# Optimization experiments

Measured on AMD Instinct MI355X. Metric: run time of the kernel, lower is better.

Reference implementation:

```python
import jax, jax.numpy as jnp
import numpy as np

B, T, DIM, H, DH = 4, 2048, 1024, 16, 64
NEG = -1.0e9


def setup_inputs() -> dict:
    key = jax.random.key(0)
    ks = jax.random.split(key, 12)
    inner = H * DH
    s_in = 1.0 / np.sqrt(DIM)
    s_out = 1.0 / np.sqrt(inner)
    q = jax.random.normal(ks[0], (B, T, DIM), jnp.float32)
    k = jax.random.normal(ks[1], (B, T, DIM), jnp.float32)
    v = jax.random.normal(ks[2], (B, T, DIM), jnp.float32)
    # nn.Linear weights stored as [out, in]; we keep [in, out] for x @ W
    W_q = jax.random.uniform(ks[3], (DIM, inner), jnp.float32, -s_in, s_in)
    b_q = jax.random.uniform(ks[4], (inner,), jnp.float32, -s_in, s_in)
    W_k = jax.random.uniform(ks[5], (DIM, inner), jnp.float32, -s_in, s_in)
    b_k = jax.random.uniform(ks[6], (inner,), jnp.float32, -s_in, s_in)
    W_v = jax.random.uniform(ks[7], (DIM, inner), jnp.float32, -s_in, s_in)
    b_v = jax.random.uniform(ks[8], (inner,), jnp.float32, -s_in, s_in)
    W_o = jax.random.uniform(ks[9], (inner, DIM), jnp.float32, -s_out, s_out)
    b_o = jax.random.uniform(ks[10], (DIM,), jnp.float32, -s_out, s_out)
    # causal mask: True = masked (strict upper triangle), broadcastable [1,1,T,T]
    causal_mask = jnp.triu(jnp.ones((T, T), bool), k=1)[None, None]
    # context mask: True = keep; random padding pattern with col 0 always valid
    context_mask = jax.random.bernoulli(ks[11], 0.9, (B, T)).at[:, 0].set(True)
    return {"q": q, "k": k, "v": v,
            "W_q": W_q, "b_q": b_q, "W_k": W_k, "b_k": b_k,
            "W_v": W_v, "b_v": b_v, "W_o": W_o, "b_o": b_o,
            "causal_mask": causal_mask, "context_mask": context_mask}


def reference(q, k, v, W_q, b_q, W_k, b_k, W_v, b_v, W_o, b_o,
              causal_mask, context_mask):
    scale = DH ** -0.5
    split = lambda x: x.reshape(x.shape[0], x.shape[1], H, DH).transpose(0, 2, 1, 3)
    qh = split(q @ W_q + b_q)  # [b,h,t,d]
    kh = split(k @ W_k + b_k)
    vh = split(v @ W_v + b_v)
    scores = jnp.einsum('bhid,bhjd->bhij', qh * scale, kh)
    scores = jnp.where(context_mask[:, None, None, :], scores, NEG)
    scores = jnp.where(causal_mask, NEG, scores)
    probs = jax.nn.softmax(scores, axis=-1)
    out = jnp.einsum('bhij,bhjd->bhid', probs, vh)
    out = out.transpose(0, 2, 1, 3).reshape(B, T, H * DH)
    return out @ W_o + b_o
```

## Files before the change

kernel.cpp:

```cpp
#include <hip/hip_runtime.h>
#include <hip/hip_bf16.h>
#include <cstdint>
#include <cstddef>

#define DEV static __device__ __forceinline__

typedef __attribute__((ext_vector_type(8))) short short8;
typedef __attribute__((ext_vector_type(4))) short short4v;
typedef __attribute__((ext_vector_type(4))) float floatx4;

#define BB 4
#define TT 2048
#define DIMM 1024
#define HH 16
#define DHH 64
#define MM (BB*TT)
#define QBLK 128
#define NQT (TT/QBLK)
#define M0F 12.0f

DEV unsigned short f2bu(float f) {
    unsigned int u = __float_as_uint(f);
    unsigned int r = (u + 0x7fffu + ((u >> 16) & 1u)) >> 16;
    return (unsigned short)r;
}

DEV unsigned long long pack4(float a, float b, float c, float d) {
    return (unsigned long long)f2bu(a) | ((unsigned long long)f2bu(b) << 16) |
           ((unsigned long long)f2bu(c) << 32) | ((unsigned long long)f2bu(d) << 48);
}

DEV unsigned int pk2(float lo, float hi) {
    __hip_bfloat162 h = __float22bfloat162_rn(make_float2(lo, hi));
    unsigned int r;
    __builtin_memcpy(&r, &h, 4);
    return r;
}

DEV unsigned long long pk4(float a, float b, float c, float d) {
    return (unsigned long long)pk2(a, b) | ((unsigned long long)pk2(c, d) << 32);
}

DEV void gload16(const void* g, void* l) {
    __builtin_amdgcn_global_load_lds(
        (const __attribute__((address_space(1))) unsigned int*)g,
        (__attribute__((address_space(3))) unsigned int*)l, 16, 0, 0);
}

#define MFMA16(a, b, c) __builtin_amdgcn_mfma_f32_16x16x32_bf16((a), (b), (c), 0, 0, 0)

#if defined(__has_builtin)
#if __has_builtin(__builtin_amdgcn_mfma_f32_16x16x16bf16_1k)
#define HAVE_MFMA_K16 1
#endif
#endif

DEV floatx4 mfma_k16(short4v a, short4v b, floatx4 c) {
#ifdef HAVE_MFMA_K16
    return __builtin_amdgcn_mfma_f32_16x16x16bf16_1k(a, b, c, 0, 0, 0);
#else
    asm volatile("v_mfma_f32_16x16x16_bf16 %0, %1, %2, %0" : "+v"(c) : "v"(a), "v"(b));
    return c;
#endif
}

__global__ __launch_bounds__(256) void ctx_bias(const unsigned char* __restrict__ raw,
                                                float* __restrict__ out) {
    __shared__ int nz1, nz23;
    if (threadIdx.x == 0) { nz1 = 0; nz23 = 0; }
    __syncthreads();
    int a1 = 0, a23 = 0;
    for (int i = threadIdx.x; i < BB * TT; i += 256) {
        unsigned char vb = raw[i];
        int m = i & 3;
        if (vb) { if (m == 1) a1 = 1; else if (m >= 2) a23 = 1; }
    }
    if (a1) atomicOr(&nz1, 1);
    if (a23) atomicOr(&nz23, 1);
    __syncthreads();
    const int mode = nz1 ? 2 : (nz23 ? 1 : 0);
    for (int i = threadIdx.x; i < BB * TT; i += 256) {
        bool keep;
        if (mode == 2)      keep = raw[i] != 0;
        else if (mode == 0) keep = raw[(size_t)4 * i] != 0;
        else                keep = (raw[(size_t)4 * i + 2] | raw[(size_t)4 * i + 3]) != 0;
        out[i] = keep ? -M0F : -3.0e38f;
    }
}

__global__ __launch_bounds__(256) void wtrans(const float* __restrict__ W0, const float* __restrict__ W1,
                                              const float* __restrict__ W2, const float* __restrict__ W3,
                                              unsigned short* __restrict__ out) {
    const float* W = blockIdx.y == 0 ? W0 : blockIdx.y == 1 ? W1 : blockIdx.y == 2 ? W2 : W3;
    unsigned short* O = out + (size_t)blockIdx.y * DIMM * DIMM;
    const int tx = blockIdx.x & 15, ty = blockIdx.x >> 4;
    __shared__ float s[64][65];
    const int tid = threadIdx.x;
#pragma unroll
    for (int j = 0; j < 4; ++j) {
        int c = tid + 256 * j;
        int r = c >> 4, c4 = c & 15;
        float4 vv = *reinterpret_cast<const float4*>(&W[(size_t)(ty * 64 + r) * DIMM + tx * 64 + c4 * 4]);
        s[r][c4 * 4 + 0] = vv.x; s[r][c4 * 4 + 1] = vv.y;
        s[r][c4 * 4 + 2] = vv.z; s[r][c4 * 4 + 3] = vv.w;
    }
    __syncthreads();
#pragma unroll
    for (int j = 0; j < 4; ++j) {
        int c = tid + 256 * j;
        int n = c >> 4, k4 = c & 15;
        unsigned long long pk = pack4(s[k4 * 4 + 0][n], s[k4 * 4 + 1][n], s[k4 * 4 + 2][n], s[k4 * 4 + 3][n]);
        *reinterpret_cast<unsigned long long*>(&O[(size_t)(tx * 64 + n) * DIMM + ty * 64 + k4 * 4]) = pk;
    }
}

__global__ __launch_bounds__(256) void cvt_bf16(const float* __restrict__ in,
                                                unsigned short* __restrict__ out) {
    const size_t i = ((size_t)blockIdx.x * 256 + threadIdx.x) * 8;
    float4 a = *reinterpret_cast<const float4*>(&in[i]);
    float4 b = *reinterpret_cast<const float4*>(&in[i + 4]);
    unsigned long long lo = pk4(a.x, a.y, a.z, a.w);
    unsigned long long hi = pk4(b.x, b.y, b.z, b.w);
    ulonglong2 v; v.x = lo; v.y = hi;
    *reinterpret_cast<ulonglong2*>(&out[i]) = v;
}

template <int OMODE>
__global__ __launch_bounds__(256) void gemm_bf16(const unsigned short* __restrict__ Ab,
                                                 const unsigned short* __restrict__ Bt,
                                                 const float* __restrict__ bias,
                                                 void* __restrict__ Cp, float scale) {
    __shared__ unsigned short As[2][128 * 64];
    __shared__ unsigned short Bs[2][128 * 64];
    const int tid = threadIdx.x, lane = tid & 63, g = lane >> 4, lq = lane & 15;
    const int wid = tid >> 6;
    const int mbase = blockIdx.x * 128, nbase = blockIdx.y * 128;
    const int wm = (wid >> 1) * 64, wn = (wid & 1) * 64;
    floatx4 acc[4][4];
#pragma unroll
    for (int i = 0; i < 4; ++i)
#pragma unroll
        for (int j = 0; j < 4; ++j) acc[i][j] = (floatx4){0.f, 0.f, 0.f, 0.f};

#define STAGE(buf, k0)                                                              \
    {                                                                               \
        _Pragma("unroll")                                                           \
        for (int j = 0; j < 4; ++j) {                                               \
            const int c = j * 256 + tid;                                            \
            const int row = c >> 3, ci = c & 7;                                     \
            const int sc = ci ^ (row & 7);                                          \
            gload16(&Ab[(size_t)(mbase + row) * DIMM + (k0) + sc * 8], &As[buf][c * 8]); \
            gload16(&Bt[(size_t)(nbase + row) * DIMM + (k0) + sc * 8], &Bs[buf][c * 8]); \
        }                                                                           \
    }

    STAGE(0, 0);
    asm volatile("s_waitcnt vmcnt(0)");
    __syncthreads();
    int cur = 0;
    for (int k0 = 0; k0 < DIMM; k0 += 64) {
        if (k0 + 64 < DIMM) STAGE(cur ^ 1, k0 + 64);
#pragma unroll
        for (int kk = 0; kk < 2; ++kk) {
            short8 af[4], bf[4];
#pragma unroll
            for (int i = 0; i < 4; ++i) {
                const int ra = wm + i * 16 + lq;
                af[i] = *reinterpret_cast<const short8*>(&As[cur][ra * 64 + ((kk * 4 + g) ^ (ra & 7)) * 8]);
                const int rb = wn + i * 16 + lq;
                bf[i] = *reinterpret_cast<const short8*>(&Bs[cur][rb * 64 + ((kk * 4 + g) ^ (rb & 7)) * 8]);
            }
#pragma unroll
            for (int i = 0; i < 4; ++i)
#pragma unroll
                for (int j2 = 0; j2 < 4; ++j2)
                    acc[i][j2] = MFMA16(af[i], bf[j2], acc[i][j2]);
        }
        __syncthreads();
        cur ^= 1;
    }
#undef STAGE

#pragma unroll
    for (int i = 0; i < 4; ++i) {
#pragma unroll
        for (int j = 0; j < 4; ++j) {
            const int col = nbase + wn + j * 16 + lq;
            const float bvv = bias[col];
            const int row0 = mbase + wm + i * 16 + g * 4;
            if (OMODE == 2) {
                float* C = (float*)Cp;
#pragma unroll
                for (int r = 0; r < 4; ++r)
                    C[(size_t)(row0 + r) * DIMM + col] = acc[i][j][r] + bvv;
            } else if (OMODE == 0) {
                unsigned short* C = (unsigned short*)Cp;
#pragma unroll
                for (int r = 0; r < 4; ++r)
                    C[(size_t)(row0 + r) * DIMM + col] = f2bu((acc[i][j][r] + bvv) * scale);
            } else {
                unsigned short* C = (unsigned short*)Cp;
                const int b = row0 >> 11, t0 = row0 & (TT - 1);
                const int h = col >> 6, d = col & 63;
                unsigned long long pk = pk4(acc[i][j][0] + bvv, acc[i][j][1] + bvv,
                                            acc[i][j][2] + bvv, acc[i][j][3] + bvv);
                *reinterpret_cast<unsigned long long*>(
                    &C[((size_t)(b * HH + h) * DHH + d) * TT + t0]) = pk;
            }
        }
    }
}

__global__ __launch_bounds__(512, 4) void attn128(const unsigned short* __restrict__ Q,
                                                  const unsigned short* __restrict__ Km,
                                                  const unsigned short* __restrict__ Vt,
                                                  const float* __restrict__ ctxb,
                                                  unsigned short* __restrict__ O) {
    const int pair = blockIdx.x >> 6, h = blockIdx.x & 15, b = (blockIdx.x >> 4) & 3;
    const int tid = threadIdx.x, lane = tid & 63, g = lane >> 4, lq = lane & 15, wid = tid >> 6;

    __shared__ unsigned short Qs[QBLK * 64];
    __shared__ unsigned short Ks[2][64 * 64];
    __shared__ unsigned short Vs[2][64 * 64];

    const float* cbias = ctxb + b * TT;
    const unsigned short* Vbase = Vt + (size_t)(b * HH + h) * DHH * TT;
    const int srow = tid >> 3, sdc = tid & 7;
    const int soff = (srow * 128 + sdc * 16) ^ ((srow & 7) << 4);

    for (int part = 0; part < 2; ++part) {
        const int qt = (part == 0) ? pair : (NQT - 1 - pair);
        const int qbase = qt * QBLK;
        const size_t rowQ = (size_t)(b * TT + qbase);
        const int nkv = 2 * qt + 2;

        __syncthreads();
#pragma unroll
        for (int j = 0; j < 2; ++j) {
            int ci = j * 512 + tid;
            int row = ci >> 3, dc = ci & 7;
            *reinterpret_cast<float4*>((char*)Qs + ((row * 128 + dc * 16) ^ ((row & 7) << 4))) =
                *reinterpret_cast<const float4*>(&Q[(rowQ + row) * DIMM + h * DHH + dc * 8]);
        }
        {
            float4 k0v = *reinterpret_cast<const float4*>(&Km[(size_t)(b * TT + srow) * DIMM + h * DHH + sdc * 8]);
            float4 v0v = *reinterpret_cast<const float4*>(&Vbase[(size_t)srow * TT + sdc * 8]);
            *reinterpret_cast<float4*>((char*)Ks[0] + soff) = k0v;
            *reinterpret_cast<float4*>((char*)Vs[0] + soff) = v0v;
        }
        __syncthreads();

        short8 qf0, qf1;
        {
            const int r = wid * 16 + lq;
            const int sw = (r & 7) << 4;
            qf0 = *reinterpret_cast<const short8*>((char*)Qs + ((r * 128 + g * 16) ^ sw));
            qf1 = *reinterpret_cast<const short8*>((char*)Qs + ((r * 128 + 64 + g * 16) ^ sw));
        }

        floatx4 oacc[4];
#pragma unroll
        for (int f = 0; f < 4; ++f) oacc[f] = (floatx4){0.f, 0.f, 0.f, 0.f};
        float l_run = 0.f;
        const int qwave_min = qbase + wid * 16;
        const int qg = qwave_min + lq;

        for (int kt = 0; kt < nkv; ++kt) {
            const int cur = kt & 1;
            const int kvb = kt * 64;
            const bool pf = (kt + 1 < nkv);
            float4 kreg, vreg;
            if (pf) {
                const int kvn = kvb + 64;
                kreg = *reinterpret_cast<const float4*>(&Km[(size_t)(b * TT + kvn + srow) * DIMM + h * DHH + sdc * 8]);
                vreg = *reinterpret_cast<const float4*>(&Vbase[(size_t)srow * TT + kvn + sdc * 8]);
            }
            if (kvb <= qwave_min + 15) {
                const bool needC = (kvb + 63 > qwave_min);
                float p[4][4];
                __builtin_amdgcn_s_setprio(1);
#pragma unroll
                for (int f = 0; f < 4; ++f) {
                    const int r = f * 16 + lq;
                    const int sw = (r & 7) << 4;
                    short8 kf0 = *reinterpret_cast<const short8*>((char*)Ks[cur] + ((r * 128 + g * 16) ^ sw));
                    short8 kf1 = *reinterpret_cast<const short8*>((char*)Ks[cur] + ((r * 128 + 64 + g * 16) ^ sw));
                    const float4 bias = *reinterpret_cast<const float4*>(&cbias[kvb + f * 16 + g * 4]);
                    floatx4 t = (floatx4){bias.x, bias.y, bias.z, bias.w};
                    t = MFMA16(kf0, qf0, t);
                    t = MFMA16(kf1, qf1, t);
#pragma unroll
                    for (int r2 = 0; r2 < 4; ++r2) {
                        float sv = t[r2];
                        if (needC) {
                            const int kv = kvb + f * 16 + g * 4 + r2;
                            if (kv > qg) sv = -3.0e38f;
                        }
                        p[f][r2] = exp2f(sv);
                    }
                }
                __builtin_amdgcn_s_setprio(0);
                float rs = 0.f;
#pragma unroll
                for (int f = 0; f < 4; ++f)
#pragma unroll
                    for (int r2 = 0; r2 < 4; ++r2) rs += p[f][r2];
                rs += __shfl_xor(rs, 16, 64);
                rs += __shfl_xor(rs, 32, 64);
                l_run += rs;
                short4v w[4];
#pragma unroll
                for (int f = 0; f < 4; ++f) {
                    unsigned long long pw = pk4(p[f][0], p[f][1], p[f][2], p[f][3]);
                    __builtin_memcpy(&w[f], &pw, 8);
                }
                __builtin_amdgcn_s_setprio(1);
#pragma unroll
                for (int f = 0; f < 4; ++f) {
                    const int r = f * 16 + lq;
                    const int sw = (r & 7) << 4;
                    const int rb = r * 128;
#pragma unroll
                    for (int j = 0; j < 4; ++j) {
                        short4v av = *reinterpret_cast<const short4v*>(
                            (char*)Vs[cur] + ((rb + j * 32 + g * 8) ^ sw));
                        oacc[f] = mfma_k16(av, w[j], oacc[f]);
                    }
                }
                __builtin_amdgcn_s_setprio(0);
#ifndef HAVE_MFMA_K16
                asm volatile("s_nop 7\ns_nop 7");
#endif
            }
            if (pf) {
                *reinterpret_cast<float4*>((char*)Ks[cur ^ 1] + soff) = kreg;
                *reinterpret_cast<float4*>((char*)Vs[cur ^ 1] + soff) = vreg;
            }
            __syncthreads();
        }

        const float inv = 1.f / l_run;
#pragma unroll
        for (int f = 0; f < 4; ++f) {
            unsigned long long pk = pk4(oacc[f][0] * inv, oacc[f][1] * inv,
                                        oacc[f][2] * inv, oacc[f][3] * inv);
            *reinterpret_cast<unsigned long long*>(
                &O[(rowQ + wid * 16 + lq) * DIMM + h * DHH + f * 16 + g * 4]) = pk;
        }
    }
}

extern "C" void kernel_launch(void* const* d_in, const int* in_sizes, int n_in,
                              void* d_out, int out_size, void* d_ws, size_t ws_size,
                              hipStream_t stream) {
    const float* q  = (const float*)d_in[0];
    const float* k  = (const float*)d_in[1];
    const float* v  = (const float*)d_in[2];
    const float* Wq = (const float*)d_in[3];
    const float* bq = (const float*)d_in[4];
    const float* Wk = (const float*)d_in[5];
    const float* bk = (const float*)d_in[6];
    const float* Wv = (const float*)d_in[7];
    const float* bv = (const float*)d_in[8];
    const float* Wo = (const float*)d_in[9];
    const float* bo = (const float*)d_in[10];
    const unsigned char* cmask = (const unsigned char*)d_in[12];

    unsigned short* Qp  = (unsigned short*)d_ws;
    unsigned short* Kp  = Qp + (size_t)MM * DIMM;
    unsigned short* Vtp = Kp + (size_t)MM * DIMM;
    unsigned short* AO  = Vtp + (size_t)MM * DIMM;
    unsigned short* Wt  = AO + (size_t)MM * DIMM;
    float* ctxb = (float*)(Wt + (size_t)4 * DIMM * DIMM);

    ctx_bias<<<dim3(1), dim3(256), 0, stream>>>(cmask, ctxb);
    wtrans<<<dim3(256, 4), dim3(256), 0, stream>>>(Wq, Wk, Wv, Wo, Wt);

    const float scale_q = 0.125f * 1.4426950408889634f;

    cvt_bf16<<<dim3(4096), dim3(256), 0, stream>>>(q, AO);
    gemm_bf16<0><<<dim3(64, 8), dim3(256), 0, stream>>>(AO, Wt,                           bq, Qp,  scale_q);
    cvt_bf16<<<dim3(4096), dim3(256), 0, stream>>>(k, AO);
    gemm_bf16<0><<<dim3(64, 8), dim3(256), 0, stream>>>(AO, Wt + (size_t)DIMM * DIMM,     bk, Kp,  1.f);
    cvt_bf16<<<dim3(4096), dim3(256), 0, stream>>>(v, AO);
    gemm_bf16<1><<<dim3(64, 8), dim3(256), 0, stream>>>(AO, Wt + (size_t)2 * DIMM * DIMM, bv, Vtp, 1.f);

    attn128<<<dim3(BB * HH * 8), dim3(512), 0, stream>>>(Qp, Kp, Vtp, ctxb, AO);

    gemm_bf16<2><<<dim3(64, 8), dim3(256), 0, stream>>>(AO, Wt + (size_t)3 * DIMM * DIMM, bo, d_out, 1.f);
}
```

Measured before the change: 224.2 us.

## Split attention into one block per query tile with longest-first ordering

The attention kernel no longer pairs two causal query tiles per block. It now launches one block per (batch, head, query tile) and orders the tiles so that the longest causal tiles are dispatched first, in a snake pattern. Q fragments are loaded straight from global memory into registers, which removes the Q shared-memory stage and one barrier. The launch-bounds occupancy hint goes from 4 to 8. This gives more blocks and finer load balancing, at the cost of relying on the dispatch order to balance the causal workload and possibly more register pressure under the higher occupancy target.

```diff
diff --git a/kernel.cpp b/kernel.cpp
--- a/kernel.cpp
+++ b/kernel.cpp
@@ -211,15 +211,17 @@
     }
 }
 
-__global__ __launch_bounds__(512, 4) void attn128(const unsigned short* __restrict__ Q,
+__global__ __launch_bounds__(512, 8) void attn128(const unsigned short* __restrict__ Q,
                                                   const unsigned short* __restrict__ Km,
                                                   const unsigned short* __restrict__ Vt,
                                                   const float* __restrict__ ctxb,
                                                   unsigned short* __restrict__ O) {
-    const int pair = blockIdx.x >> 6, h = blockIdx.x & 15, b = (blockIdx.x >> 4) & 3;
+    const int bh = blockIdx.x & 63, qtIdx = blockIdx.x >> 6;
+    const int h = bh & 15, b = bh >> 4;
+    const int jj = qtIdx >> 2, ii = qtIdx & 3;
+    const int qt = jj == 0 ? 15 - ii : jj == 1 ? 8 + ii : jj == 2 ? 7 - ii : ii;
     const int tid = threadIdx.x, lane = tid & 63, g = lane >> 4, lq = lane & 15, wid = tid >> 6;
 
-    __shared__ unsigned short Qs[QBLK * 64];
     __shared__ unsigned short Ks[2][64 * 64];
     __shared__ unsigned short Vs[2][64 * 64];
 
@@ -228,125 +230,109 @@
     const int srow = tid >> 3, sdc = tid & 7;
     const int soff = (srow * 128 + sdc * 16) ^ ((srow & 7) << 4);
 
-    for (int part = 0; part < 2; ++part) {
-        const int qt = (part == 0) ? pair : (NQT - 1 - pair);
-        const int qbase = qt * QBLK;
-        const size_t rowQ = (size_t)(b * TT + qbase);
-        const int nkv = 2 * qt + 2;
-
+    const int qbase = qt * QBLK;
+    const size_t rowQ = (size_t)(b * TT + qbase);
+    const int nkv = 2 * qt + 2;
+
+    {
+        float4 k0v = *reinterpret_cast<const float4*>(&Km[(size_t)(b * TT + srow) * DIMM + h * DHH + sdc * 8]);
+        float4 v0v = *reinterpret_cast<const float4*>(&Vbase[(size_t)srow * TT + sdc * 8]);
+        *reinterpret_cast<float4*>((char*)Ks[0] + soff) = k0v;
+        *reinterpret_cast<float4*>((char*)Vs[0] + soff) = v0v;
+    }
+    const int qrow = wid * 16 + lq;
+    short8 qf0 = *reinterpret_cast<const short8*>(&Q[(rowQ + qrow) * DIMM + h * DHH + g * 8]);
+    short8 qf1 = *reinterpret_cast<const short8*>(&Q[(rowQ + qrow) * DIMM + h * DHH + 32 + g * 8]);
+    __syncthreads();
+
+    floatx4 oacc[4];
+#pragma unroll
+    for (int f = 0; f < 4; ++f) oacc[f] = (floatx4){0.f, 0.f, 0.f, 0.f};
+    float l_run = 0.f;
+    const int qwave_min = qbase + wid * 16;
+    const int qg = qwave_min + lq;
+
+    for (int kt = 0; kt < nkv; ++kt) {
+        const int cur = kt & 1;
+        const int kvb = kt * 64;
+        const bool pf = (kt + 1 < nkv);
+        float4 kreg, vreg;
+        if (pf) {
+            const int kvn = kvb + 64;
+            kreg = *reinterpret_cast<const float4*>(&Km[(size_t)(b * TT + kvn + srow) * DIMM + h * DHH + sdc * 8]);
+            vreg = *reinterpret_cast<const float4*>(&Vbase[(size_t)srow * TT + kvn + sdc * 8]);
+        }
+        if (kvb <= qwave_min + 15) {
+            const bool needC = (kvb + 63 > qwave_min);
+            float p[4][4];
+            __builtin_amdgcn_s_setprio(1);
+#pragma unroll
+            for (int f = 0; f < 4; ++f) {
+                const int r = f * 16 + lq;
+                const int sw = (r & 7) << 4;
+                short8 kf0 = *reinterpret_cast<const short8*>((char*)Ks[cur] + ((r * 128 + g * 16) ^ sw));
+                short8 kf1 = *reinterpret_cast<const short8*>((char*)Ks[cur] + ((r * 128 + 64 + g * 16) ^ sw));
+                const float4 bias = *reinterpret_cast<const float4*>(&cbias[kvb + f * 16 + g * 4]);
+                floatx4 t = (floatx4){bias.x, bias.y, bias.z, bias.w};
+                t = MFMA16(kf0, qf0, t);
+                t = MFMA16(kf1, qf1, t);
+#pragma unroll
+                for (int r2 = 0; r2 < 4; ++r2) {
+                    float sv = t[r2];
+                    if (needC) {
+                        const int kv = kvb + f * 16 + g * 4 + r2;
+                        if (kv > qg) sv = -3.0e38f;
+                    }
+                    p[f][r2] = exp2f(sv);
+                }
+            }
+            __builtin_amdgcn_s_setprio(0);
+            float rs = 0.f;
+#pragma unroll
+            for (int f = 0; f < 4; ++f)
+#pragma unroll
+                for (int r2 = 0; r2 < 4; ++r2) rs += p[f][r2];
+            rs += __shfl_xor(rs, 16, 64);
+            rs += __shfl_xor(rs, 32, 64);
+            l_run += rs;
+            short4v w[4];
+#pragma unroll
+            for (int f = 0; f < 4; ++f) {
+                unsigned long long pw = pk4(p[f][0], p[f][1], p[f][2], p[f][3]);
+                __builtin_memcpy(&w[f], &pw, 8);
+            }
+            __builtin_amdgcn_s_setprio(1);
+#pragma unroll
+            for (int f = 0; f < 4; ++f) {
+                const int r = f * 16 + lq;
+                const int sw = (r & 7) << 4;
+                const int rb = r * 128;
+#pragma unroll
+                for (int j = 0; j < 4; ++j) {
+                    short4v av = *reinterpret_cast<const short4v*>(
+                        (char*)Vs[cur] + ((rb + j * 32 + g * 8) ^ sw));
+                    oacc[f] = mfma_k16(av, w[j], oacc[f]);
+                }
+            }
+            __builtin_amdgcn_s_setprio(0);
+#ifndef HAVE_MFMA_K16
+            asm volatile("s_nop 7\ns_nop 7");
+#endif
+        }
+        if (pf) {
+            *reinterpret_cast<float4*>((char*)Ks[cur ^ 1] + soff) = kreg;
+            *reinterpret_cast<float4*>((char*)Vs[cur ^ 1] + soff) = vreg;
+        }
         __syncthreads();
-#pragma unroll
-        for (int j = 0; j < 2; ++j) {
-            int ci = j * 512 + tid;
-            int row = ci >> 3, dc = ci & 7;
-            *reinterpret_cast<float4*>((char*)Qs + ((row * 128 + dc * 16) ^ ((row & 7) << 4))) =
-                *reinterpret_cast<const float4*>(&Q[(rowQ + row) * DIMM + h * DHH + dc * 8]);
-        }
-        {
-            float4 k0v = *reinterpret_cast<const float4*>(&Km[(size_t)(b * TT + srow) * DIMM + h * DHH + sdc * 8]);
-            float4 v0v = *reinterpret_cast<const float4*>(&Vbase[(size_t)srow * TT + sdc * 8]);
-            *reinterpret_cast<float4*>((char*)Ks[0] + soff) = k0v;
-            *reinterpret_cast<float4*>((char*)Vs[0] + soff) = v0v;
-        }
-        __syncthreads();
-
-        short8 qf0, qf1;
-        {
-            const int r = wid * 16 + lq;
-            const int sw = (r & 7) << 4;
-            qf0 = *reinterpret_cast<const short8*>((char*)Qs + ((r * 128 + g * 16) ^ sw));
-            qf1 = *reinterpret_cast<const short8*>((char*)Qs + ((r * 128 + 64 + g * 16) ^ sw));
-        }
-
-        floatx4 oacc[4];
-#pragma unroll
-        for (int f = 0; f < 4; ++f) oacc[f] = (floatx4){0.f, 0.f, 0.f, 0.f};
-        float l_run = 0.f;
-        const int qwave_min = qbase + wid * 16;
-        const int qg = qwave_min + lq;
-
-        for (int kt = 0; kt < nkv; ++kt) {
-            const int cur = kt & 1;
-            const int kvb = kt * 64;
-            const bool pf = (kt + 1 < nkv);
-            float4 kreg, vreg;
-            if (pf) {
-                const int kvn = kvb + 64;
-                kreg = *reinterpret_cast<const float4*>(&Km[(size_t)(b * TT + kvn + srow) * DIMM + h * DHH + sdc * 8]);
-                vreg = *reinterpret_cast<const float4*>(&Vbase[(size_t)srow * TT + kvn + sdc * 8]);
-            }
-            if (kvb <= qwave_min + 15) {
-                const bool needC = (kvb + 63 > qwave_min);
-                float p[4][4];
-                __builtin_amdgcn_s_setprio(1);
-#pragma unroll
-                for (int f = 0; f < 4; ++f) {
-                    const int r = f * 16 + lq;
-                    const int sw = (r & 7) << 4;
-                    short8 kf0 = *reinterpret_cast<const short8*>((char*)Ks[cur] + ((r * 128 + g * 16) ^ sw));
-                    short8 kf1 = *reinterpret_cast<const short8*>((char*)Ks[cur] + ((r * 128 + 64 + g * 16) ^ sw));
-                    const float4 bias = *reinterpret_cast<const float4*>(&cbias[kvb + f * 16 + g * 4]);
-                    floatx4 t = (floatx4){bias.x, bias.y, bias.z, bias.w};
-                    t = MFMA16(kf0, qf0, t);
-                    t = MFMA16(kf1, qf1, t);
-#pragma unroll
-                    for (int r2 = 0; r2 < 4; ++r2) {
-                        float sv = t[r2];
-                        if (needC) {
-                            const int kv = kvb + f * 16 + g * 4 + r2;
-                            if (kv > qg) sv = -3.0e38f;
-                        }
-                        p[f][r2] = exp2f(sv);
-                    }
-                }
-                __builtin_amdgcn_s_setprio(0);
-                float rs = 0.f;
-#pragma unroll
-                for (int f = 0; f < 4; ++f)
-#pragma unroll
-                    for (int r2 = 0; r2 < 4; ++r2) rs += p[f][r2];
-                rs += __shfl_xor(rs, 16, 64);
-                rs += __shfl_xor(rs, 32, 64);
-                l_run += rs;
-                short4v w[4];
-#pragma unroll
-                for (int f = 0; f < 4; ++f) {
-                    unsigned long long pw = pk4(p[f][0], p[f][1], p[f][2], p[f][3]);
-                    __builtin_memcpy(&w[f], &pw, 8);
-                }
-                __builtin_amdgcn_s_setprio(1);
-#pragma unroll
-                for (int f = 0; f < 4; ++f) {
-                    const int r = f * 16 + lq;
-                    const int sw = (r & 7) << 4;
-                    const int rb = r * 128;
-#pragma unroll
-                    for (int j = 0; j < 4; ++j) {
-                        short4v av = *reinterpret_cast<const short4v*>(
-                            (char*)Vs[cur] + ((rb + j * 32 + g * 8) ^ sw));
-                        oacc[f] = mfma_k16(av, w[j], oacc[f]);
-                    }
-                }
-                __builtin_amdgcn_s_setprio(0);
-#ifndef HAVE_MFMA_K16
-                asm volatile("s_nop 7\ns_nop 7");
-#endif
-            }
-            if (pf) {
-                *reinterpret_cast<float4*>((char*)Ks[cur ^ 1] + soff) = kreg;
-                *reinterpret_cast<float4*>((char*)Vs[cur ^ 1] + soff) = vreg;
-            }
-            __syncthreads();
-        }
-
-        const float inv = 1.f / l_run;
-#pragma unroll
-        for (int f = 0; f < 4; ++f) {
-            unsigned long long pk = pk4(oacc[f][0] * inv, oacc[f][1] * inv,
-                                        oacc[f][2] * inv, oacc[f][3] * inv);
-            *reinterpret_cast<unsigned long long*>(
-                &O[(rowQ + wid * 16 + lq) * DIMM + h * DHH + f * 16 + g * 4]) = pk;
-        }
+    }
+
+    const float inv = 1.f / l_run;
+#pragma unroll
+    for (int f = 0; f < 4; ++f) {
+        unsigned long long pk = pk4(oacc[f][0] * inv, oacc[f][1] * inv,
+                                    oacc[f][2] * inv, oacc[f][3] * inv);
+        *reinterpret_cast<unsigned long long*>(
+            &O[(rowQ + qrow) * DIMM + h * DHH + f * 16 + g * 4]) = pk;
     }
 }
 
@@ -385,7 +371,7 @@
     cvt_bf16<<<dim3(4096), dim3(256), 0, stream>>>(v, AO);
     gemm_bf16<1><<<dim3(64, 8), dim3(256), 0, stream>>>(AO, Wt + (size_t)2 * DIMM * DIMM, bv, Vtp, 1.f);
 
-    attn128<<<dim3(BB * HH * 8), dim3(512), 0, stream>>>(Qp, Kp, Vtp, ctxb, AO);
+    attn128<<<dim3(BB * HH * NQT), dim3(512), 0, stream>>>(Qp, Kp, Vtp, ctxb, AO);
 
     gemm_bf16<2><<<dim3(64, 8), dim3(256), 0, stream>>>(AO, Wt + (size_t)3 * DIMM * DIMM, bo, d_out, 1.f);
 }
```

Result: slower. 493.2 us (+120.0%).
